# Kernel optimization log

Measured on AMD Instinct MI355X. Metric: run time of the kernel, lower is better.

The kernel has to match this reference:

```python
import jax, jax.numpy as jnp
import numpy as np

B, T, C = 4, 1024, 1024
N = 64          # head_size
H = C // N      # 16 heads
DW, DA, DV, DG = 64, 64, 64, 160


def setup_inputs() -> dict:
    key = jax.random.key(0)
    ks = iter(jax.random.split(key, 40))
    rn = lambda shape, s=1.0: jax.random.normal(next(ks), shape, dtype=jnp.float32) * s
    ru = lambda shape: jax.random.uniform(next(ks), shape, dtype=jnp.float32)
    cs = 0.5 / (C ** 0.5)
    return {
        "x": rn((B, T, C)),
        "v_first": rn((B, T, C)),
        "x_r": ru((1, 1, C)), "x_w": ru((1, 1, C)), "x_k": ru((1, 1, C)),
        "x_v": ru((1, 1, C)), "x_a": ru((1, 1, C)), "x_g": ru((1, 1, C)),
        "w0": rn((1, 1, C), 0.3) - 1.0,
        "w1": rn((C, DW), 0.05), "w2": rn((DW, C), 0.05),
        "a0": rn((1, 1, C), 0.3) - 0.19,
        "a1": rn((C, DA), 0.05), "a2": rn((DA, C), 0.05),
        "v0": rn((1, 1, C), 0.3) + 0.73,
        "v1": rn((C, DV), 0.05), "v2": rn((DV, C), 0.05),
        "g1": rn((C, DG), 0.05), "g2": rn((DG, C), 0.05),
        "k_k": ru((1, 1, C)) * 0.2 + 0.6,
        "k_a": ru((1, 1, C)) * 0.2 + 0.9,
        "r_k": rn((H, N), 0.05) - 0.04,
        "Wr": rn((C, C), cs), "Wk": rn((C, C), 0.1 * cs),
        "Wv": rn((C, C), cs), "Wo": rn((C, C), 0.02),
        "gn_w": jnp.ones((C,), jnp.float32), "gn_b": jnp.zeros((C,), jnp.float32),
        "ln_w": jnp.ones((C,), jnp.float32), "ln_b": jnp.zeros((C,), jnp.float32),
    }


def reference(x, v_first, x_r, x_w, x_k, x_v, x_a, x_g,
              w0, w1, w2, a0, a1, a2, v0, v1, v2, g1, g2,
              k_k, k_a, r_k, Wr, Wk, Wv, Wo, gn_w, gn_b, ln_w, ln_b):
    Bb, Tt, Cc = x.shape
    # ZeroPad2d((0,0,1,-1)): shift tokens right by one along T, then subtract x
    xx = jnp.concatenate([jnp.zeros_like(x[:, :1]), x[:, :-1]], axis=1) - x
    xr = x + xx * x_r; xw = x + xx * x_w; xkk = x + xx * x_k
    xv = x + xx * x_v; xa = x + xx * x_a; xg = x + xx * x_g

    r = xr @ Wr.T                                                    # [B,T,C]
    w = -jax.nn.softplus(-(w0 + jnp.tanh(xw @ w1) @ w2)) - 0.5       # log-decay <= -0.5
    k = xkk @ Wk.T
    v = xv @ Wv.T
    # layer_id=1 != 0 -> value residual mixing with v_first
    v = v + (v_first - v) * jax.nn.sigmoid(v0 + (xv @ v1) @ v2)
    a = jax.nn.sigmoid(a0 + (xa @ a1) @ a2)
    g = jax.nn.sigmoid(xg @ g1) @ g2

    kk = (k * k_k).reshape(Bb, Tt, H, N)
    kk = kk / jnp.maximum(jnp.linalg.norm(kk, axis=-1, keepdims=True), 1e-12)
    kk = kk.reshape(Bb, Tt, Cc)
    k = k * (1.0 + (a - 1.0) * k_a)

    # RWKV-7 generalized delta rule scan: kernel args (r, w, k, v, -kk, kk*a)
    decay = jnp.exp(-jnp.exp(w))                                     # [B,T,C]
    aa = -kk
    bb = kk * a
    tbhn = lambda t: t.reshape(Bb, Tt, H, N).transpose(1, 0, 2, 3)   # [T,B,H,N]
    rs, ws, ks_, vs, as_, bs = map(tbhn, (r, decay, k, v, aa, bb))

    S0 = jnp.zeros((Bb, H, N, N), dtype=x.dtype)  # [B,H, value N, key N]

    def step(S, inp):
        r_t, w_t, k_t, v_t, a_t, b_t = inp
        sa = jnp.einsum('bhij,bhj->bhi', S, a_t)                     # removal readout
        S = (S * w_t[:, :, None, :]
             + sa[..., None] * b_t[:, :, None, :]
             + v_t[..., None] * k_t[:, :, None, :])
        y = jnp.einsum('bhij,bhj->bhi', S, r_t)
        return S, (y, sa)

    _, (ys, sas) = jax.lax.scan(step, S0, (rs, ws, ks_, vs, as_, bs))
    x_att = ys.transpose(1, 0, 2, 3).reshape(Bb, Tt, Cc)
    sa_out = sas.transpose(1, 0, 2, 3).reshape(Bb, Tt, Cc)

    # ln_sa: LayerNorm over C (eps 1e-5)
    mu = sa_out.mean(-1, keepdims=True)
    var = sa_out.var(-1, keepdims=True)
    state_rep = (sa_out - mu) / jnp.sqrt(var + 1e-5) * ln_w + ln_b

    # ln_x: GroupNorm(H groups, eps=0.00064) applied per token
    xh = x_att.reshape(Bb, Tt, H, N)
    gm = xh.mean(-1, keepdims=True)
    gv = xh.var(-1, keepdims=True)
    xn = ((xh - gm) / jnp.sqrt(gv + 0.00064)).reshape(Bb, Tt, Cc) * gn_w + gn_b

    rh = r.reshape(Bb, Tt, H, N)
    kh = k.reshape(Bb, Tt, H, N)
    vh = v.reshape(Bb, Tt, H, N)
    bonus = ((rh * kh * r_k).sum(-1, keepdims=True) * vh).reshape(Bb, Tt, Cc)
    x_att = xn + bonus

    out = (x_att * g) @ Wo.T
    return out, v_first, state_rep
```

## Files before the change

kernel.cpp:

```cpp
#include <hip/hip_runtime.h>
#include <hip/hip_bf16.h>
#include <cstdint>
#include <cstddef>

typedef __attribute__((ext_vector_type(8))) short short8;
typedef __attribute__((ext_vector_type(4))) short short4v;
typedef __attribute__((ext_vector_type(4))) float f32x4;

#define DEVINL static __device__ __forceinline__

DEVINL float b2f(unsigned short u) {
    union { unsigned int i; float f; } v; v.i = ((unsigned int)u) << 16; return v.f;
}
DEVINL unsigned short f2b(float f) {
    union { float f; unsigned int i; } v; v.f = f;
    unsigned int x = v.i;
    return (unsigned short)((x + 0x7FFFu + ((x >> 16) & 1u)) >> 16);
}
DEVINL unsigned short f2bh(float f) {
    __hip_bfloat16 h = __float2bfloat16(f);
    union { __hip_bfloat16 h; unsigned short u; } v; v.h = h; return v.u;
}
DEVINL void cv8(short8 h, f32x4& lo, f32x4& hi) {
    #pragma unroll
    for (int j = 0; j < 4; ++j) {
        lo[j] = b2f((unsigned short)h[j]);
        hi[j] = b2f((unsigned short)h[j + 4]);
    }
}
DEVINL void cv4(short4v h, f32x4& o) {
    #pragma unroll
    for (int j = 0; j < 4; ++j) o[j] = b2f((unsigned short)h[j]);
}
DEVINL void stage16(const unsigned short* g, unsigned short* l) {
    __builtin_amdgcn_global_load_lds(
        (const __attribute__((address_space(1))) unsigned int*)g,
        (__attribute__((address_space(3))) unsigned int*)l,
        16, 0, 0);
}
DEVINL void xcd_swz(int& bx, int& by) {
    int id = by * 32 + bx;
    int nid = (id & 7) * 32 + (id >> 3);
    bx = nid & 31; by = nid >> 5;
}

static constexpr int Bsz = 4, Tn = 1024, Cn = 1024, Hn = 16, Nn = 64;
static constexpr int Mrows = Bsz * Tn;
static constexpr size_t MX = (size_t)Mrows * Cn;
static constexpr int NCHUNK = 16, CL = 64;
static constexpr int DLD = 65;

__global__ __launch_bounds__(256) void k_prep_all(
    const float* __restrict__ x,
    const float* __restrict__ mr, const float* __restrict__ mw,
    const float* __restrict__ mk, const float* __restrict__ mv,
    const float* __restrict__ ma, const float* __restrict__ mg,
    unsigned short* __restrict__ xr, unsigned short* __restrict__ xw,
    unsigned short* __restrict__ xk, unsigned short* __restrict__ xv,
    unsigned short* __restrict__ xa, unsigned short* __restrict__ xg,
    const float* __restrict__ Wr, const float* __restrict__ Wk,
    const float* __restrict__ Wv, const float* __restrict__ Wo,
    unsigned short* __restrict__ WrB, unsigned short* __restrict__ WkB,
    unsigned short* __restrict__ WvB, unsigned short* __restrict__ WoB,
    const float* __restrict__ w1, const float* __restrict__ w2,
    const float* __restrict__ a1, const float* __restrict__ a2,
    const float* __restrict__ v1, const float* __restrict__ v2,
    const float* __restrict__ g1, const float* __restrict__ g2,
    unsigned short* __restrict__ w1T, unsigned short* __restrict__ w2T,
    unsigned short* __restrict__ a1T, unsigned short* __restrict__ a2T,
    unsigned short* __restrict__ v1T, unsigned short* __restrict__ v2T,
    unsigned short* __restrict__ g1T, unsigned short* __restrict__ g2T)
{
    const int bx = blockIdx.x;
    const int tid = threadIdx.x;
    if (bx < 2048) {
        size_t e = ((size_t)bx * 256 + tid) * 8;
        int c = (int)(e & (Cn - 1));
        int t = (int)((e >> 10) & (Tn - 1));
        float xf[8], d[8];
        {
            f32x4 x0 = *(const f32x4*)(x + e);
            f32x4 x1 = *(const f32x4*)(x + e + 4);
            #pragma unroll
            for (int j = 0; j < 4; ++j) { xf[j] = x0[j]; xf[4 + j] = x1[j]; }
        }
        if (t > 0) {
            f32x4 p0 = *(const f32x4*)(x + e - Cn);
            f32x4 p1 = *(const f32x4*)(x + e - Cn + 4);
            #pragma unroll
            for (int j = 0; j < 4; ++j) { d[j] = p0[j] - xf[j]; d[4 + j] = p1[j] - xf[4 + j]; }
        } else {
            #pragma unroll
            for (int j = 0; j < 8; ++j) d[j] = -xf[j];
        }
        const float* ms[6] = { mr, mw, mk, mv, ma, mg };
        unsigned short* ds[6] = { xr, xw, xk, xv, xa, xg };
        #pragma unroll
        for (int p = 0; p < 6; ++p) {
            f32x4 m0 = *(const f32x4*)(ms[p] + c);
            f32x4 m1 = *(const f32x4*)(ms[p] + c + 4);
            short8 o;
            #pragma unroll
            for (int j = 0; j < 4; ++j) {
                o[j]     = (short)f2b(xf[j]     + d[j]     * m0[j]);
                o[4 + j] = (short)f2b(xf[4 + j] + d[4 + j] * m1[j]);
            }
            *(short8*)(ds[p] + e) = o;
        }
    } else if (bx < 6144) {
        int b2 = bx - 2048;
        int sel = b2 >> 10;
        const float* in = (sel == 0) ? Wr : (sel == 1) ? Wk : (sel == 2) ? Wv : Wo;
        unsigned short* out = (sel == 0) ? WrB : (sel == 1) ? WkB : (sel == 2) ? WvB : WoB;
        int i = (((b2 & 1023) << 8) + tid) * 4;
        f32x4 v = *(const f32x4*)(in + i);
        short4v o;
        #pragma unroll
        for (int j = 0; j < 4; ++j) o[j] = (short)f2b(v[j]);
        *(short4v*)(out + i) = o;
    } else {
        int idx = (bx - 6144) * 256 + tid;
        if (idx < 65536) {
            int r = idx >> 6, c = idx & 63;
            w1T[c * 1024 + r] = f2b(w1[idx]);
        } else if (idx < 131072) {
            int j = idx - 65536; int r = j >> 10, c = j & 1023;
            w2T[c * 64 + r] = f2b(w2[j]);
        } else if (idx < 196608) {
            int j = idx - 131072; int r = j >> 6, c = j & 63;
            a1T[c * 1024 + r] = f2b(a1[j]);
        } else if (idx < 262144) {
            int j = idx - 196608; int r = j >> 10, c = j & 1023;
            a2T[c * 64 + r] = f2b(a2[j]);
        } else if (idx < 327680) {
            int j = idx - 262144; int r = j >> 6, c = j & 63;
            v1T[c * 1024 + r] = f2b(v1[j]);
        } else if (idx < 393216) {
            int j = idx - 327680; int r = j >> 10, c = j & 1023;
            v2T[c * 64 + r] = f2b(v2[j]);
        } else if (idx < 557056) {
            int j = idx - 393216; int r = j / 160, c = j - r * 160;
            g1T[c * 1024 + r] = f2b(g1[j]);
        } else if (idx < 720896) {
            int j = idx - 557056; int r = j >> 10, c = j & 1023;
            g2T[c * 160 + r] = f2b(g2[j]);
        }
    }
}

template<int EPI, int OUTF32>
DEVINL void gemm_epi(f32x4 (&acc)[4][4], int m0, int n0, int N, int ldc,
                     float* Cf, unsigned short* Cb, const float* bias, int lane)
{
    int r16 = lane & 15;
    #pragma unroll
    for (int mi = 0; mi < 4; ++mi)
        #pragma unroll
        for (int ni = 0; ni < 4; ++ni) {
            int col = n0 + ni * 16 + r16;
            if (col < N) {
                float bv = (EPI >= 3) ? bias[col] : 0.f;
                #pragma unroll
                for (int r = 0; r < 4; ++r) {
                    int row = m0 + mi * 16 + (lane >> 4) * 4 + r;
                    float v = acc[mi][ni][r];
                    if (EPI == 1) v = tanhf(v);
                    else if (EPI == 2) v = 1.f / (1.f + expf(-v));
                    else if (EPI == 3) { v += bv; v = 1.f / (1.f + expf(-v)); }
                    else if (EPI == 4) { v += bv; v = expf(-0.60653066f / (1.f + expf(-v))); }
                    size_t o = (size_t)row * ldc + col;
                    if (OUTF32) Cf[o] = v; else Cb[o] = f2b(v);
                }
            }
        }
}

template<int EPI, int OUTF32>
DEVINL void gemm_lds_body(const unsigned short* __restrict__ A, int lda,
                          const unsigned short* __restrict__ Bt, int ldb,
                          float* __restrict__ Cf, unsigned short* __restrict__ Cb,
                          int ldc, const float* __restrict__ bias, int K,
                          int m0, int n0)
{
    __shared__ unsigned short As[2][128 * 32];
    __shared__ unsigned short Bs[2][128 * 32];
    const int tid = threadIdx.x, wid = tid >> 6, lane = tid & 63;
    const int r16 = lane & 15, kg = lane >> 4;
    const int wr = (wid >> 1) * 64, wc = (wid & 1) * 64;

    const int srow = wid * 32 + (lane >> 2);
    const int scol = (lane & 3) * 8;
    const int lbase = wid * 1024 + lane * 8;
    const unsigned short* aS = A + (size_t)(m0 + srow) * lda + scol;
    const unsigned short* bS = Bt + (size_t)(n0 + srow) * ldb + scol;

    f32x4 acc[4][4];
    #pragma unroll
    for (int a = 0; a < 4; ++a)
        #pragma unroll
        for (int b = 0; b < 4; ++b) acc[a][b] = (f32x4){0.f, 0.f, 0.f, 0.f};

    const int nk = K >> 5;
    stage16(aS, &As[0][lbase]);
    stage16(aS + (size_t)16 * lda, &As[0][lbase + 512]);
    stage16(bS, &Bs[0][lbase]);
    stage16(bS + (size_t)16 * ldb, &Bs[0][lbase + 512]);
    __syncthreads();

    for (int kk = 0; kk < nk; ++kk) {
        const int buf = kk & 1;
        if (kk + 1 < nk) {
            const int k0 = (kk + 1) * 32;
            stage16(aS + k0, &As[buf ^ 1][lbase]);
            stage16(aS + k0 + (size_t)16 * lda, &As[buf ^ 1][lbase + 512]);
            stage16(bS + k0, &Bs[buf ^ 1][lbase]);
            stage16(bS + k0 + (size_t)16 * ldb, &Bs[buf ^ 1][lbase + 512]);
        }
        short8 af[4], bf[4];
        #pragma unroll
        for (int mi = 0; mi < 4; ++mi)
            af[mi] = *(const short8*)&As[buf][(wr + mi * 16 + r16) * 32 + kg * 8];
        #pragma unroll
        for (int ni = 0; ni < 4; ++ni)
            bf[ni] = *(const short8*)&Bs[buf][(wc + ni * 16 + r16) * 32 + kg * 8];
        #pragma unroll
        for (int mi = 0; mi < 4; ++mi)
            #pragma unroll
            for (int ni = 0; ni < 4; ++ni)
                acc[mi][ni] = __builtin_amdgcn_mfma_f32_16x16x32_bf16(af[mi], bf[ni], acc[mi][ni], 0, 0, 0);
        __syncthreads();
    }
    gemm_epi<EPI, OUTF32>(acc, m0 + wr, n0 + wc, 1 << 30, ldc, Cf, Cb, bias, lane);
}

__global__ __launch_bounds__(256) void gemm_rkv(
    const unsigned short* __restrict__ A0, const unsigned short* __restrict__ A1,
    const unsigned short* __restrict__ A2,
    const unsigned short* __restrict__ B0, const unsigned short* __restrict__ B1,
    const unsigned short* __restrict__ B2,
    unsigned short* __restrict__ D0, unsigned short* __restrict__ D1,
    unsigned short* __restrict__ D2)
{
    int z = blockIdx.z;
    const unsigned short* A = (z == 0) ? A0 : (z == 1) ? A1 : A2;
    const unsigned short* Bt = (z == 0) ? B0 : (z == 1) ? B1 : B2;
    unsigned short* D = (z == 0) ? D0 : (z == 1) ? D1 : D2;
    int bxs = blockIdx.x, bys = blockIdx.y;
    xcd_swz(bxs, bys);
    gemm_lds_body<0, 0>(A, Cn, Bt, Cn, nullptr, D, Cn, nullptr, Cn,
                        bxs * 128, bys * 128);
}

__global__ __launch_bounds__(256) void gemm_s2(
    const unsigned short* __restrict__ hw, const unsigned short* __restrict__ ha,
    const unsigned short* __restrict__ hv, const unsigned short* __restrict__ hg,
    const unsigned short* __restrict__ w2T, const unsigned short* __restrict__ a2T,
    const unsigned short* __restrict__ v2T, const unsigned short* __restrict__ g2T,
    float* __restrict__ Wdec, unsigned short* __restrict__ Ab,
    unsigned short* __restrict__ SVb, unsigned short* __restrict__ Gb,
    const float* __restrict__ w0, const float* __restrict__ a0,
    const float* __restrict__ v0)
{
    const int z = blockIdx.z;
    int bxs = blockIdx.x, bys = blockIdx.y;
    xcd_swz(bxs, bys);
    const int m0 = bxs * 128, n0 = bys * 128;
    if (z == 0)
        gemm_lds_body<4, 1>(hw, 64, w2T, 64, Wdec, nullptr, Cn, w0, 64, m0, n0);
    else if (z == 1)
        gemm_lds_body<3, 0>(ha, 64, a2T, 64, nullptr, Ab, Cn, a0, 64, m0, n0);
    else if (z == 2)
        gemm_lds_body<3, 0>(hv, 64, v2T, 64, nullptr, SVb, Cn, v0, 64, m0, n0);
    else
        gemm_lds_body<0, 0>(hg, 160, g2T, 160, nullptr, Gb, Cn, nullptr, 160, m0, n0);
}

template<int EPI, int OUTF32>
__global__ __launch_bounds__(256) void gemm2(
    const unsigned short* __restrict__ A, int lda,
    const unsigned short* __restrict__ Bt, int ldb,
    float* __restrict__ Cf, unsigned short* __restrict__ Cb, int ldc,
    const float* __restrict__ bias, int K)
{
    int bxs = blockIdx.x, bys = blockIdx.y;
    xcd_swz(bxs, bys);
    gemm_lds_body<EPI, OUTF32>(A, lda, Bt, ldb, Cf, Cb, ldc, bias, K,
                               bxs * 128, bys * 128);
}

DEVINL void gemm_core(const unsigned short* __restrict__ A, int lda,
                      const unsigned short* __restrict__ Bt, int ldb,
                      int m0, int n0, int N, int K, int r16, int k8,
                      f32x4 (&acc)[4][4])
{
    for (int k0 = 0; k0 < K; k0 += 32) {
        short8 af[4], bf[4];
        #pragma unroll
        for (int mi = 0; mi < 4; ++mi)
            af[mi] = *(const short8*)(A + (size_t)(m0 + mi * 16 + r16) * lda + k0 + k8);
        #pragma unroll
        for (int ni = 0; ni < 4; ++ni) {
            int rn = n0 + ni * 16 + r16;
            if (rn >= N) rn = N - 1;
            bf[ni] = *(const short8*)(Bt + (size_t)rn * ldb + k0 + k8);
        }
        #pragma unroll
        for (int mi = 0; mi < 4; ++mi)
            #pragma unroll
            for (int ni = 0; ni < 4; ++ni)
                acc[mi][ni] = __builtin_amdgcn_mfma_f32_16x16x32_bf16(af[mi], bf[ni], acc[mi][ni], 0, 0, 0);
    }
}

__global__ __launch_bounds__(256) void gemm_small1(
    const unsigned short* __restrict__ Aw, const unsigned short* __restrict__ Aa,
    const unsigned short* __restrict__ Av, const unsigned short* __restrict__ Ag,
    const unsigned short* __restrict__ Bw, const unsigned short* __restrict__ Ba,
    const unsigned short* __restrict__ Bv, const unsigned short* __restrict__ Bg,
    unsigned short* __restrict__ Dw, unsigned short* __restrict__ Da,
    unsigned short* __restrict__ Dv, unsigned short* __restrict__ Dg)
{
    int z = blockIdx.z;
    if (z < 3 && blockIdx.y > 0) return;
    const unsigned short* A = (z == 0) ? Aw : (z == 1) ? Aa : (z == 2) ? Av : Ag;
    const unsigned short* Bt = (z == 0) ? Bw : (z == 1) ? Ba : (z == 2) ? Bv : Bg;
    const int N = (z == 3) ? 160 : 64;
    const int tid = threadIdx.x, wid = tid >> 6, lane = tid & 63;
    const int r16 = lane & 15, k8 = (lane >> 4) * 8;
    const int m0 = blockIdx.x * 256 + wid * 64;
    const int n0 = blockIdx.y * 64;
    f32x4 acc[4][4];
    #pragma unroll
    for (int a = 0; a < 4; ++a)
        #pragma unroll
        for (int b = 0; b < 4; ++b) acc[a][b] = (f32x4){0.f, 0.f, 0.f, 0.f};
    gemm_core(A, Cn, Bt, Cn, m0, n0, N, Cn, r16, k8, acc);
    if (z == 0)      gemm_epi<1, 0>(acc, m0, n0, N, 64,  nullptr, Dw, nullptr, lane);
    else if (z == 1) gemm_epi<0, 0>(acc, m0, n0, N, 64,  nullptr, Da, nullptr, lane);
    else if (z == 2) gemm_epi<0, 0>(acc, m0, n0, N, 64,  nullptr, Dv, nullptr, lane);
    else             gemm_epi<2, 0>(acc, m0, n0, N, 160, nullptr, Dg, nullptr, lane);
}

__global__ __launch_bounds__(1024, 1) void kA_wy(
    const float* __restrict__ Wp,
    unsigned short* __restrict__ Kp,
    unsigned short* __restrict__ Vp,
    const unsigned short* __restrict__ SVp,
    unsigned short* __restrict__ Aap,
    const float* __restrict__ vfirst,
    const float* __restrict__ kkw, const float* __restrict__ kaw,
    float* __restrict__ Pg,
    float* __restrict__ Cg,
    float* __restrict__ Qg,
    float* __restrict__ SAp)
{
    __shared__ float Dl[64 * DLD];
    __shared__ float Lf[64 * 72];
    __shared__ float Xf[64 * 132];
    __shared__ unsigned short ah[64 * 72], al[64 * 72];
    __shared__ unsigned short bh_[64 * 72], bl_[64 * 72];
    __shared__ unsigned short kh[64 * 72], kl[64 * 72];
    __shared__ unsigned short vt[64 * 72];
    __shared__ unsigned short sc[64 * 72];
    __shared__ float dT[64];

    const int tid = threadIdx.x;
    const int bx = blockIdx.x;
    const int bhd = bx >> 4, cc = bx & 15;
    const size_t base0 = ((size_t)(bhd >> 4) * Tn + (size_t)cc * CL) * Cn + (size_t)(bhd & 15) * Nn;
    const size_t mb = (size_t)bx * 4096;

    {
        const int t = tid >> 4, s4 = (tid & 15) * 4;
        const size_t g = base0 + (size_t)t * Cn + s4;
        const int ch = (bhd & 15) * Nn + s4;

        f32x4 kv, av, vv, sv;
        cv4(*(const short4v*)(Kp + g), kv);
        cv4(*(const short4v*)(Aap + g), av);
        cv4(*(const short4v*)(Vp + g), vv);
        cv4(*(const short4v*)(SVp + g), sv);
        f32x4 kkwv = *(const f32x4*)(kkw + ch);
        f32x4 kawv = *(const f32x4*)(kaw + ch);
        f32x4 vfv  = *(const f32x4*)(vfirst + g);

        f32x4 kkv = kv * kkwv;
        f32x4 sq = kkv * kkv;
        float s = sq[0] + sq[1] + sq[2] + sq[3];
        s += __shfl_xor(s, 1, 64); s += __shfl_xor(s, 2, 64);
        s += __shfl_xor(s, 4, 64); s += __shfl_xor(s, 8, 64);
        float inv = 1.f / fmaxf(sqrtf(s), 1e-12f);

        short4v o_a, o_b, o_k, o_v;
        #pragma unroll
        for (int j = 0; j < 4; ++j) {
            float kkx = kkv[j] * inv;
            o_a[j] = (short)f2b(-kkx);
            o_b[j] = (short)f2b(kkx * av[j]);
            float kf = kv[j] * (1.f + (av[j] - 1.f) * kawv[j]);
            o_k[j] = (short)f2b(kf);
            float vf = vv[j] + (vfv[j] - vv[j]) * sv[j];
            o_v[j] = (short)f2b(vf);
        }
        *(short4v*)&ah[t * 72 + s4] = o_a;
        *(short4v*)&bh_[t * 72 + s4] = o_b;
        *(short4v*)&kh[t * 72 + s4] = o_k;
        *(short4v*)&sc[t * 72 + s4] = o_v;
        *(short4v*)(Kp + g) = o_k;
        *(short4v*)(Vp + g) = o_v;
        *(short4v*)(Aap + g) = o_b;
    }
    __syncthreads();

    float wreg[4];
    {
        const int j = tid & 63, seg = tid >> 6;
        const float* wp = Wp + base0 + (size_t)(seg * 4) * Cn + j;
        float run = 1.f;
        #pragma unroll
        for (int u = 0; u < 4; ++u) { wreg[u] = wp[(size_t)u * Cn]; run *= wreg[u]; }
        Xf[seg * 64 + j] = run;
    }
    __syncthreads();
    {
        const int j = tid & 63, seg = tid >> 6;
        float d = 1.f;
        for (int q = 0; q < seg; ++q) d *= Xf[q * 64 + j];
        #pragma unroll
        for (int u = 0; u < 4; ++u) { d *= wreg[u]; Dl[(seg * 4 + u) * DLD + j] = d; }
        if (seg == 15) dT[j] = d;
    }
    __syncthreads();

    {
        const int t = tid >> 4, s4 = (tid & 15) * 4;
        short4v a4 = *(const short4v*)&ah[t * 72 + s4];
        short4v b4 = *(const short4v*)&bh_[t * 72 + s4];
        short4v k4 = *(const short4v*)&kh[t * 72 + s4];
        short4v oah, oal, obh, obl, okh, okl;
        #pragma unroll
        for (int jj = 0; jj < 4; ++jj) {
            const int j = s4 + jj;
            const float Dt = Dl[t * DLD + j];
            const float Dp = (t == 0) ? 1.f : Dl[(t - 1) * DLD + j];
            const float inv = __builtin_amdgcn_rcpf(Dt);
            float av = b2f((unsigned short)a4[jj]) * Dp;
            unsigned short h = f2bh(av);
            oah[jj] = (short)h; oal[jj] = (short)f2bh(av - b2f(h));
            float bv = b2f((unsigned short)b4[jj]) * inv;
            h = f2bh(bv);
            obh[jj] = (short)h; obl[jj] = (short)f2bh(bv - b2f(h));
            float kv = b2f((unsigned short)k4[jj]) * inv;
            h = f2bh(kv);
            okh[jj] = (short)h; okl[jj] = (short)f2bh(kv - b2f(h));
        }
        *(short4v*)&ah[t * 72 + s4] = oah;  *(short4v*)&al[t * 72 + s4] = oal;
        *(short4v*)&bh_[t * 72 + s4] = obh; *(short4v*)&bl_[t * 72 + s4] = obl;
        *(short4v*)&kh[t * 72 + s4] = okh;  *(short4v*)&kl[t * 72 + s4] = okl;
    }
    {
        const int rj = tid & 63, tq = tid >> 6;
        short4v ov;
        #pragma unroll
        for (int u = 0; u < 4; ++u)
            ov[u] = (short)sc[(tq * 4 + u) * 72 + rj];
        *(short4v*)&vt[rj * 72 + tq * 4] = ov;
    }
    __syncthreads();

    const int w = tid >> 6, lane = tid & 63;
    const int r16 = lane & 15, kg = lane >> 4;
    const int rt = w >> 2, ct = w & 3;

    {
        if (ct > rt) {
            #pragma unroll
            for (int r = 0; r < 4; ++r)
                sc[(rt * 16 + kg * 4 + r) * 72 + ct * 16 + r16] = 0;
        } else {
            short8 Ah[2], Al2[2];
            #pragma unroll
            for (int ks = 0; ks < 2; ++ks) {
                Ah[ks]  = *(const short8*)&ah[(rt * 16 + r16) * 72 + ks * 32 + kg * 8];
                Al2[ks] = *(const short8*)&al[(rt * 16 + r16) * 72 + ks * 32 + kg * 8];
            }
            f32x4 aL = (f32x4){0.f, 0.f, 0.f, 0.f};
            f32x4 aK = (f32x4){0.f, 0.f, 0.f, 0.f};
            #pragma unroll
            for (int ks = 0; ks < 2; ++ks) {
                const int so = (ct * 16 + r16) * 72 + ks * 32 + kg * 8;
                short8 Bh = *(const short8*)&bh_[so];
                short8 Bl = *(const short8*)&bl_[so];
                aL = __builtin_amdgcn_mfma_f32_16x16x32_bf16(Ah[ks], Bh, aL, 0, 0, 0);
                aL = __builtin_amdgcn_mfma_f32_16x16x32_bf16(Ah[ks], Bl, aL, 0, 0, 0);
                aL = __builtin_amdgcn_mfma_f32_16x16x32_bf16(Al2[ks], Bh, aL, 0, 0, 0);
                short8 Kh2 = *(const short8*)&kh[so];
                short8 Kl2 = *(const short8*)&kl[so];
                aK = __builtin_amdgcn_mfma_f32_16x16x32_bf16(Ah[ks], Kh2, aK, 0, 0, 0);
                aK = __builtin_amdgcn_mfma_f32_16x16x32_bf16(Ah[ks], Kl2, aK, 0, 0, 0);
                aK = __builtin_amdgcn_mfma_f32_16x16x32_bf16(Al2[ks], Kh2, aK, 0, 0, 0);
            }
            #pragma unroll
            for (int r = 0; r < 4; ++r) {
                const int t = rt * 16 + kg * 4 + r;
                const int s = ct * 16 + r16;
                Lf[t * 72 + s] = (s < t) ? aL[r] : 0.f;
                sc[t * 72 + s] = (s < t) ? f2bh(aK[r]) : (unsigned short)0;
            }
        }
    }
    __syncthreads();

    {
        const int t = tid >> 4, s4 = (tid & 15) * 4;
        #pragma unroll
        for (int jj = 0; jj < 4; ++jj)
            Xf[t * 132 + s4 + jj] = b2f(ah[t * 72 + s4 + jj]) + b2f(al[t * 72 + s4 + jj]);
    }
    {
        f32x4 acc = (f32x4){0.f, 0.f, 0.f, 0.f};
        #pragma unroll
        for (int ks = 0; ks < 2; ++ks) {
            short8 Af = *(const short8*)&sc[(rt * 16 + r16) * 72 + ks * 32 + kg * 8];
            short8 Bf = *(const short8*)&vt[(ct * 16 + r16) * 72 + ks * 32 + kg * 8];
            acc = __builtin_amdgcn_mfma_f32_16x16x32_bf16(Af, Bf, acc, 0, 0, 0);
        }
        #pragma unroll
        for (int r = 0; r < 4; ++r)
            Xf[(rt * 16 + kg * 4 + r) * 132 + 64 + ct * 16 + r16] = acc[r];
    }
    __syncthreads();

    for (int bi = 0; bi < 4; ++bi) {
        if (bi > 0) {
            const int c = tid & 127;
            const int rb = tid >> 7;
            const int t0 = bi * 16 + rb * 2;
            float a0 = Xf[t0 * 132 + c];
            float a1 = Xf[(t0 + 1) * 132 + c];
            for (int s = 0; s < bi * 16; ++s) {
                float xv = Xf[s * 132 + c];
                a0 += Lf[t0 * 72 + s] * xv;
                a1 += Lf[(t0 + 1) * 72 + s] * xv;
            }
            Xf[t0 * 132 + c] = a0;
            Xf[(t0 + 1) * 132 + c] = a1;
            __syncthreads();
        }
        if (w < 2) {
            const int c = w * 64 + lane;
            float xcol[16];
            #pragma unroll
            for (int u = 0; u < 16; ++u) xcol[u] = Xf[(bi * 16 + u) * 132 + c];
            for (int rr = 1; rr < 16; ++rr) {
                float a2 = xcol[rr];
                for (int s = 0; s < rr; ++s)
                    a2 += Lf[(bi * 16 + rr) * 72 + bi * 16 + s] * xcol[s];
                xcol[rr] = a2;
            }
            #pragma unroll
            for (int u = 1; u < 16; ++u) Xf[(bi * 16 + u) * 132 + c] = xcol[u];
        }
        __syncthreads();
    }

    {
        const int rj = tid & 63, tq = tid >> 6;
        float qv[4], sv[4];
        unsigned short bhv[4], blv[4], khv[4], klv[4];
        #pragma unroll
        for (int u = 0; u < 4; ++u) {
            const int t = tq * 4 + u;
            qv[u] = Xf[t * 132 + rj];
            sv[u] = Xf[t * 132 + 64 + rj];
            bhv[u] = bh_[t * 72 + rj];
            blv[u] = bl_[t * 72 + rj];
            khv[u] = kh[t * 72 + rj];
            klv[u] = kl[t * 72 + rj];
        }
        #pragma unroll
        for (int u = 0; u < 4; ++u) {
            const int t = tq * 4 + u;
            Qg[mb + (size_t)t * 64 + rj] = qv[u];
            SAp[base0 + (size_t)t * Cn + rj] = sv[u];
        }
        __syncthreads();
        unsigned short* sath = (unsigned short*)Lf;
        unsigned short* satl = ((unsigned short*)Lf) + 64 * 72;
        short4v oqh, oql, osh, osl, obh, obl, okh, okl;
        #pragma unroll
        for (int u = 0; u < 4; ++u) {
            unsigned short h = f2bh(qv[u]);
            oqh[u] = (short)h; oql[u] = (short)f2bh(qv[u] - b2f(h));
            h = f2bh(sv[u]);
            osh[u] = (short)h; osl[u] = (short)f2bh(sv[u] - b2f(h));
            obh[u] = (short)bhv[u]; obl[u] = (short)blv[u];
            okh[u] = (short)khv[u]; okl[u] = (short)klv[u];
        }
        *(short4v*)&ah[rj * 72 + tq * 4] = oqh;
        *(short4v*)&al[rj * 72 + tq * 4] = oql;
        *(short4v*)&sath[rj * 72 + tq * 4] = osh;
        *(short4v*)&satl[rj * 72 + tq * 4] = osl;
        *(short4v*)&bh_[rj * 72 + tq * 4] = obh;
        *(short4v*)&bl_[rj * 72 + tq * 4] = obl;
        *(short4v*)&kh[rj * 72 + tq * 4] = okh;
        *(short4v*)&kl[rj * 72 + tq * 4] = okl;
    }
    __syncthreads();

    {
        unsigned short* sath = (unsigned short*)Lf;
        unsigned short* satl = ((unsigned short*)Lf) + 64 * 72;
        f32x4 aP = (f32x4){0.f, 0.f, 0.f, 0.f};
        f32x4 aC = (f32x4){0.f, 0.f, 0.f, 0.f};
        #pragma unroll
        for (int ks = 0; ks < 2; ++ks) {
            const int ro = (rt * 16 + r16) * 72 + ks * 32 + kg * 8;
            const int co = (ct * 16 + r16) * 72 + ks * 32 + kg * 8;
            short8 Abh = *(const short8*)&bh_[ro];
            short8 Abl = *(const short8*)&bl_[ro];
            short8 Bqh = *(const short8*)&ah[co];
            short8 Bql = *(const short8*)&al[co];
            aP = __builtin_amdgcn_mfma_f32_16x16x32_bf16(Abh, Bqh, aP, 0, 0, 0);
            aP = __builtin_amdgcn_mfma_f32_16x16x32_bf16(Abh, Bql, aP, 0, 0, 0);
            aP = __builtin_amdgcn_mfma_f32_16x16x32_bf16(Abl, Bqh, aP, 0, 0, 0);
            short8 Ash = *(const short8*)&sath[ro];
            short8 Asl = *(const short8*)&satl[ro];
            short8 Bbh = *(const short8*)&bh_[co];
            short8 Bbl = *(const short8*)&bl_[co];
            aC = __builtin_amdgcn_mfma_f32_16x16x32_bf16(Ash, Bbh, aC, 0, 0, 0);
            aC = __builtin_amdgcn_mfma_f32_16x16x32_bf16(Ash, Bbl, aC, 0, 0, 0);
            aC = __builtin_amdgcn_mfma_f32_16x16x32_bf16(Asl, Bbh, aC, 0, 0, 0);
            short8 Avt = *(const short8*)&vt[ro];
            short8 Bkh = *(const short8*)&kh[co];
            short8 Bkl = *(const short8*)&kl[co];
            aC = __builtin_amdgcn_mfma_f32_16x16x32_bf16(Avt, Bkh, aC, 0, 0, 0);
            aC = __builtin_amdgcn_mfma_f32_16x16x32_bf16(Avt, Bkl, aC, 0, 0, 0);
        }
        #pragma unroll
        for (int r = 0; r < 4; ++r) {
            const int row = rt * 16 + kg * 4 + r;
            const int col = ct * 16 + r16;
            Pg[mb + (size_t)row * 64 + col] = dT[row] * (aP[r] + ((row == col) ? 1.f : 0.f));
            Cg[mb + (size_t)row * 64 + col] = dT[col] * aC[r];
        }
    }
}

__global__ __launch_bounds__(256, 1) void kB_combine(
    const float* __restrict__ Pg, const float* __restrict__ Cg,
    float* __restrict__ Sinit)
{
    __shared__ float Sl[64 * 65];
    __shared__ float PT[64 * 65];
    const int tid = threadIdx.x;
    const int w = tid >> 6;
    const int l = tid & 63;
    const int lr = l & 15;
    const int lg = l >> 4;
    const int bh = blockIdx.x;

    f32x4 acc[4];
    #pragma unroll
    for (int t = 0; t < 4; ++t) acc[t] = (f32x4){0.f, 0.f, 0.f, 0.f};

    f32x4 pr[4]; f32x4 cr[4];
    {
        const size_t ob = (size_t)(bh * 16) * 4096;
        #pragma unroll
        for (int u = 0; u < 4; ++u)
            pr[u] = *(const f32x4*)(Pg + ob + (size_t)tid * 16 + u * 4);
        #pragma unroll
        for (int t = 0; t < 4; ++t)
            #pragma unroll
            for (int r = 0; r < 4; ++r)
                cr[t][r] = Cg[ob + (size_t)(16 * w + 4 * lg + r) * 64 + 16 * t + lr];
    }

    for (int c = 0; c < NCHUNK; ++c) {
        const size_t ob = (size_t)(bh * 16 + c) * 4096;
        #pragma unroll
        for (int t = 0; t < 4; ++t)
            #pragma unroll
            for (int r = 0; r < 4; ++r)
                Sinit[ob + (size_t)(16 * w + 4 * lg + r) * 64 + 16 * t + lr] = acc[t][r];
        if (c == NCHUNK - 1) break;

        #pragma unroll
        for (int t = 0; t < 4; ++t)
            #pragma unroll
            for (int r = 0; r < 4; ++r)
                Sl[(16 * w + 4 * lg + r) * 65 + 16 * t + lr] = acc[t][r];
        {
            const int jr = tid >> 2, j0 = (tid & 3) * 16;
            #pragma unroll
            for (int u = 0; u < 4; ++u)
                #pragma unroll
                for (int e = 0; e < 4; ++e)
                    PT[jr * 65 + j0 + u * 4 + e] = pr[u][e];
        }
        __syncthreads();

        f32x4 prn[4] = {}, crn[4] = {};
        if (c + 1 < NCHUNK - 1) {
            const size_t obn = (size_t)(bh * 16 + c + 1) * 4096;
            #pragma unroll
            for (int u = 0; u < 4; ++u)
                prn[u] = *(const f32x4*)(Pg + obn + (size_t)tid * 16 + u * 4);
            #pragma unroll
            for (int t = 0; t < 4; ++t)
                #pragma unroll
                for (int r = 0; r < 4; ++r)
                    crn[t][r] = Cg[obn + (size_t)(16 * w + 4 * lg + r) * 64 + 16 * t + lr];
        }

        short8 ahi[2], alo[2];
        #pragma unroll
        for (int k0 = 0; k0 < 2; ++k0) {
            const float* sp = &Sl[(16 * w + lr) * 65 + k0 * 32 + lg * 8];
            #pragma unroll
            for (int j = 0; j < 8; ++j) {
                float s = sp[j];
                unsigned short h = f2bh(s);
                ahi[k0][j] = (short)h;
                alo[k0][j] = (short)f2bh(s - b2f(h));
            }
        }

        #pragma unroll
        for (int t = 0; t < 4; ++t) {
            f32x4 nacc = cr[t];
            #pragma unroll
            for (int k0 = 0; k0 < 2; ++k0) {
                short8 bhi, blo;
                const float* pp = &PT[(16 * t + lr) * 65 + k0 * 32 + lg * 8];
                #pragma unroll
                for (int j = 0; j < 8; ++j) {
                    float p = pp[j];
                    unsigned short h = f2bh(p);
                    bhi[j] = (short)h;
                    blo[j] = (short)f2bh(p - b2f(h));
                }
                nacc = __builtin_amdgcn_mfma_f32_16x16x32_bf16(ahi[k0], bhi, nacc, 0, 0, 0);
                nacc = __builtin_amdgcn_mfma_f32_16x16x32_bf16(ahi[k0], blo, nacc, 0, 0, 0);
                nacc = __builtin_amdgcn_mfma_f32_16x16x32_bf16(alo[k0], bhi, nacc, 0, 0, 0);
            }
            acc[t] = nacc;
        }
        __syncthreads();
        #pragma unroll
        for (int u = 0; u < 4; ++u) { pr[u] = prn[u]; cr[u] = crn[u]; }
    }
}

__global__ __launch_bounds__(256) void kY_mfma(
    const float* __restrict__ Wp, const unsigned short* __restrict__ Rp,
    const unsigned short* __restrict__ Kp, const unsigned short* __restrict__ Bbp,
    const unsigned short* __restrict__ Vp,
    const float* __restrict__ Qg, const float* __restrict__ Sinit,
    float* __restrict__ SAp,
    float* __restrict__ Yp)
{
    __shared__ float Dl[64 * DLD];
    __shared__ unsigned short khS[64 * 72], klS[64 * 72];
    __shared__ unsigned short bhS[64 * 72], blS[64 * 72];
    __shared__ unsigned short vtS[64 * 72];
    __shared__ unsigned short sahS[64 * 72];

    unsigned short* scoreS = (unsigned short*)Dl;
    float* SAf = Dl;
    float* segP = (float*)vtS;

    const int tid = threadIdx.x;
    const int bx = blockIdx.x;
    const int bh = bx >> 4, cc = bx & 15;
    const size_t base0 = ((size_t)(bh >> 4) * Tn + (size_t)cc * CL) * Cn + (size_t)(bh & 15) * Nn;
    const size_t mb = (size_t)bx * 4096;

    float wv[16];
    {
        const int j = tid & 63, seg = tid >> 6;
        float run = 1.f;
        #pragma unroll
        for (int u = 0; u < 16; ++u) {
            wv[u] = Wp[base0 + (size_t)(seg * 16 + u) * Cn + j];
            run *= wv[u];
        }
        segP[seg * 64 + j] = run;
    }
    __syncthreads();
    {
        const int j = tid & 63, seg = tid >> 6;
        float d = 1.f;
        for (int q = 0; q < seg; ++q) d *= segP[q * 64 + j];
        #pragma unroll
        for (int u = 0; u < 16; ++u) {
            d *= wv[u];
            Dl[(seg * 16 + u) * DLD + j] = d;
        }
    }
    __syncthreads();

    const int w = tid >> 6, lane = tid & 63;
    const int r16 = lane & 15, kg = lane >> 4;

    short8 rh[2], rl[2];
    {
        const int t = 16 * w + r16;
        #pragma unroll
        for (int ks = 0; ks < 2; ++ks) {
            const int j0 = ks * 32 + kg * 8;
            short8 rr = *(const short8*)(Rp + base0 + (size_t)t * Cn + j0);
            const float* dp = &Dl[t * DLD + j0];
            #pragma unroll
            for (int jj = 0; jj < 8; ++jj) {
                float rv = b2f((unsigned short)rr[jj]) * dp[jj];
                unsigned short h = f2bh(rv);
                rh[ks][jj] = (short)h;
                rl[ks][jj] = (short)f2bh(rv - b2f(h));
            }
        }
    }

    {
        const int s = tid >> 2, j0 = (tid & 3) * 16;
        const size_t g = base0 + (size_t)s * Cn + j0;
        #pragma unroll
        for (int half = 0; half < 2; ++half) {
            short8 kk8 = *(const short8*)(Kp + g + half * 8);
            short8 bb8 = *(const short8*)(Bbp + g + half * 8);
            short8 okh, okl, obh, obl;
            #pragma unroll
            for (int jj = 0; jj < 8; ++jj) {
                float dd = Dl[s * DLD + j0 + half * 8 + jj];
                float inv = __builtin_amdgcn_rcpf(dd);
                float kv = b2f((unsigned short)kk8[jj]) * inv;
                float bv = b2f((unsigned short)bb8[jj]) * inv;
                unsigned short h1 = f2bh(kv);
                okh[jj] = (short)h1; okl[jj] = (short)f2bh(kv - b2f(h1));
                unsigned short h2 = f2bh(bv);
                obh[jj] = (short)h2; obl[jj] = (short)f2bh(bv - b2f(h2));
            }
            *(short8*)&khS[s * 72 + j0 + half * 8] = okh;
            *(short8*)&klS[s * 72 + j0 + half * 8] = okl;
            *(short8*)&bhS[s * 72 + j0 + half * 8] = obh;
            *(short8*)&blS[s * 72 + j0 + half * 8] = obl;
            *(short8*)&sahS[s * 72 + j0 + half * 8] =
                *(const short8*)(Vp + g + half * 8);
        }
    }
    __syncthreads();

    {
        const int rj = tid & 63, tq = tid >> 6;
        unsigned short tmp[16];
        #pragma unroll
        for (int u = 0; u < 16; ++u)
            tmp[u] = sahS[(tq * 16 + u) * 72 + rj];
        short8 o0, o1;
        #pragma unroll
        for (int u = 0; u < 8; ++u) { o0[u] = (short)tmp[u]; o1[u] = (short)tmp[8 + u]; }
        *(short8*)&vtS[rj * 72 + tq * 16] = o0;
        *(short8*)&vtS[rj * 72 + tq * 16 + 8] = o1;
    }
    __syncthreads();

    f32x4 acc[4], accC[4];
    #pragma unroll
    for (int ni = 0; ni < 4; ++ni) {
        acc[ni] = (f32x4){0.f, 0.f, 0.f, 0.f};
        accC[ni] = (f32x4){0.f, 0.f, 0.f, 0.f};
    }
    short8 qh[2], ql[2];
    if (cc > 0) {
        const int t = 16 * w + r16;
        #pragma unroll
        for (int ks = 0; ks < 2; ++ks) {
            const int j0 = ks * 32 + kg * 8;
            f32x4 qa = *(const f32x4*)(Qg + mb + (size_t)t * 64 + j0);
            f32x4 qb = *(const f32x4*)(Qg + mb + (size_t)t * 64 + j0 + 4);
            #pragma unroll
            for (int jj = 0; jj < 4; ++jj) {
                unsigned short h1 = f2bh(qa[jj]);
                qh[ks][jj] = (short)h1; ql[ks][jj] = (short)f2bh(qa[jj] - b2f(h1));
                unsigned short h2 = f2bh(qb[jj]);
                qh[ks][4 + jj] = (short)h2; ql[ks][4 + jj] = (short)f2bh(qb[jj] - b2f(h2));
            }
        }
    }
    #pragma unroll
    for (int ni = 0; ni < 4; ++ni) {
        #pragma unroll
        for (int ks = 0; ks < 2; ++ks) {
            const int i = ni * 16 + r16;
            const int j0 = ks * 32 + kg * 8;
            f32x4 s0a = *(const f32x4*)(Sinit + mb + (size_t)i * 64 + j0);
            f32x4 s0b = *(const f32x4*)(Sinit + mb + (size_t)i * 64 + j0 + 4);
            short8 s0h, s0l;
            #pragma unroll
            for (int jj = 0; jj < 4; ++jj) {
                unsigned short h1 = f2bh(s0a[jj]);
                s0h[jj] = (short)h1; s0l[jj] = (short)f2bh(s0a[jj] - b2f(h1));
                unsigned short h2 = f2bh(s0b[jj]);
                s0h[4 + jj] = (short)h2; s0l[4 + jj] = (short)f2bh(s0b[jj] - b2f(h2));
            }
            acc[ni] = __builtin_amdgcn_mfma_f32_16x16x32_bf16(rh[ks], s0h, acc[ni], 0, 0, 0);
            acc[ni] = __builtin_amdgcn_mfma_f32_16x16x32_bf16(rh[ks], s0l, acc[ni], 0, 0, 0);
            acc[ni] = __builtin_amdgcn_mfma_f32_16x16x32_bf16(rl[ks], s0h, acc[ni], 0, 0, 0);
            if (cc > 0) {
                accC[ni] = __builtin_amdgcn_mfma_f32_16x16x32_bf16(qh[ks], s0h, accC[ni], 0, 0, 0);
                accC[ni] = __builtin_amdgcn_mfma_f32_16x16x32_bf16(qh[ks], s0l, accC[ni], 0, 0, 0);
                accC[ni] = __builtin_amdgcn_mfma_f32_16x16x32_bf16(ql[ks], s0h, accC[ni], 0, 0, 0);
            }
        }
    }

    #pragma unroll
    for (int ni = 0; ni < 4; ++ni) {
        #pragma unroll
        for (int r = 0; r < 4; ++r) {
            const int t = 16 * w + kg * 4 + r;
            const int i = ni * 16 + r16;
            const size_t off = base0 + (size_t)t * Cn + i;
            float sa = SAp[off] + accC[ni][r];
            SAp[off] = sa;
            SAf[t * 65 + i] = sa;
        }
    }
    __syncthreads();

    {
        const int rj = tid & 63, tq = tid >> 6;
        unsigned short tmp[16];
        #pragma unroll
        for (int u = 0; u < 16; ++u)
            tmp[u] = f2bh(SAf[(tq * 16 + u) * 65 + rj]);
        short8 o0, o1;
        #pragma unroll
        for (int u = 0; u < 8; ++u) { o0[u] = (short)tmp[u]; o1[u] = (short)tmp[8 + u]; }
        *(short8*)&sahS[rj * 72 + tq * 16] = o0;
        *(short8*)&sahS[rj * 72 + tq * 16 + 8] = o1;
    }
    __syncthreads();

    #pragma unroll
    for (int si = 0; si < 4; ++si) {
        f32x4 sc2 = (f32x4){0.f, 0.f, 0.f, 0.f};
        #pragma unroll
        for (int ks = 0; ks < 2; ++ks) {
            const int srow = si * 16 + r16;
            const int j0 = ks * 32 + kg * 8;
            short8 kbh = *(const short8*)&khS[srow * 72 + j0];
            short8 kbl = *(const short8*)&klS[srow * 72 + j0];
            sc2 = __builtin_amdgcn_mfma_f32_16x16x32_bf16(rh[ks], kbh, sc2, 0, 0, 0);
            sc2 = __builtin_amdgcn_mfma_f32_16x16x32_bf16(rh[ks], kbl, sc2, 0, 0, 0);
            sc2 = __builtin_amdgcn_mfma_f32_16x16x32_bf16(rl[ks], kbh, sc2, 0, 0, 0);
        }
        const int s = si * 16 + r16;
        #pragma unroll
        for (int r = 0; r < 4; ++r) {
            const int t = 16 * w + kg * 4 + r;
            scoreS[t * 72 + s] = (s <= t) ? f2bh(sc2[r]) : (unsigned short)0;
        }
    }
    #pragma unroll
    for (int ni = 0; ni < 4; ++ni) {
        #pragma unroll
        for (int ks = 0; ks < 2; ++ks) {
            short8 af = *(const short8*)&scoreS[(16 * w + r16) * 72 + ks * 32 + kg * 8];
            short8 vf = *(const short8*)&vtS[(ni * 16 + r16) * 72 + ks * 32 + kg * 8];
            acc[ni] = __builtin_amdgcn_mfma_f32_16x16x32_bf16(af, vf, acc[ni], 0, 0, 0);
        }
    }
    __syncthreads();

    #pragma unroll
    for (int si = 0; si < 4; ++si) {
        f32x4 sc2 = (f32x4){0.f, 0.f, 0.f, 0.f};
        #pragma unroll
        for (int ks = 0; ks < 2; ++ks) {
            const int srow = si * 16 + r16;
            const int j0 = ks * 32 + kg * 8;
            short8 bbh = *(const short8*)&bhS[srow * 72 + j0];
            short8 bbl = *(const short8*)&blS[srow * 72 + j0];
            sc2 = __builtin_amdgcn_mfma_f32_16x16x32_bf16(rh[ks], bbh, sc2, 0, 0, 0);
            sc2 = __builtin_amdgcn_mfma_f32_16x16x32_bf16(rh[ks], bbl, sc2, 0, 0, 0);
            sc2 = __builtin_amdgcn_mfma_f32_16x16x32_bf16(rl[ks], bbh, sc2, 0, 0, 0);
        }
        const int s = si * 16 + r16;
        #pragma unroll
        for (int r = 0; r < 4; ++r) {
            const int t = 16 * w + kg * 4 + r;
            scoreS[t * 72 + s] = (s <= t) ? f2bh(sc2[r]) : (unsigned short)0;
        }
    }
    #pragma unroll
    for (int ni = 0; ni < 4; ++ni) {
        #pragma unroll
        for (int ks = 0; ks < 2; ++ks) {
            short8 af = *(const short8*)&scoreS[(16 * w + r16) * 72 + ks * 32 + kg * 8];
            short8 sh = *(const short8*)&sahS[(ni * 16 + r16) * 72 + ks * 32 + kg * 8];
            acc[ni] = __builtin_amdgcn_mfma_f32_16x16x32_bf16(af, sh, acc[ni], 0, 0, 0);
        }
    }

    #pragma unroll
    for (int ni = 0; ni < 4; ++ni) {
        #pragma unroll
        for (int r = 0; r < 4; ++r) {
            const int t = 16 * w + kg * 4 + r;
            Yp[base0 + (size_t)t * Cn + ni * 16 + r16] = acc[ni][r];
        }
    }
}

__global__ __launch_bounds__(256) void k_elem2(
    const float* __restrict__ Yb, const unsigned short* __restrict__ Rb,
    const unsigned short* __restrict__ Kb, const unsigned short* __restrict__ Vb,
    const unsigned short* __restrict__ Gb,
    const float* __restrict__ gnw, const float* __restrict__ gnb,
    const float* __restrict__ rk,
    unsigned short* __restrict__ AG)
{
    int tid = threadIdx.x;
    size_t gh = (size_t)blockIdx.x * 4 + (tid >> 6);
    int lane = tid & 63;
    int h = (int)(gh & (Hn - 1));
    size_t idx = (gh >> 4) * Cn + (size_t)h * Nn + lane;
    int c = h * Nn + lane;

    float y = Yb[idx];
    float s1 = y, s2 = y * y;
    float p = b2f(Rb[idx]) * b2f(Kb[idx]) * rk[c];
    #pragma unroll
    for (int m = 1; m < 64; m <<= 1) {
        s1 += __shfl_xor(s1, m, 64);
        s2 += __shfl_xor(s2, m, 64);
        p  += __shfl_xor(p, m, 64);
    }
    float mean = s1 * (1.f / 64.f);
    float var = s2 * (1.f / 64.f) - mean * mean;
    float xn = (y - mean) * rsqrtf(var + 0.00064f) * gnw[c] + gnb[c];
    float xatt = xn + p * b2f(Vb[idx]);
    AG[idx] = f2b(xatt * b2f(Gb[idx]));
}

__global__ __launch_bounds__(256) void k_ln(
    const float* __restrict__ SAp,
    const float* __restrict__ lnw, const float* __restrict__ lnb,
    const float* __restrict__ vf_in, float* __restrict__ vf_out,
    float* __restrict__ outp)
{
    __shared__ float red1[4], red2[4];
    int tid = threadIdx.x;
    size_t row = blockIdx.x;
    *(f32x4*)(vf_out + row * Cn + tid * 4) = *(const f32x4*)(vf_in + row * Cn + tid * 4);

    f32x4 v = *(const f32x4*)(SAp + row * Cn + tid * 4);
    float s1 = v[0] + v[1] + v[2] + v[3];
    float s2 = v[0] * v[0] + v[1] * v[1] + v[2] * v[2] + v[3] * v[3];
    #pragma unroll
    for (int m = 1; m < 64; m <<= 1) {
        s1 += __shfl_xor(s1, m, 64);
        s2 += __shfl_xor(s2, m, 64);
    }
    if ((tid & 63) == 0) { red1[tid >> 6] = s1; red2[tid >> 6] = s2; }
    __syncthreads();
    s1 = red1[0] + red1[1] + red1[2] + red1[3];
    s2 = red2[0] + red2[1] + red2[2] + red2[3];
    float mean = s1 * (1.f / 1024.f);
    float var = s2 * (1.f / 1024.f) - mean * mean;
    float rs = rsqrtf(var + 1e-5f);
    f32x4 o;
    #pragma unroll
    for (int u = 0; u < 4; ++u) {
        int c = tid * 4 + u;
        o[u] = (v[u] - mean) * rs * lnw[c] + lnb[c];
    }
    *(f32x4*)(outp + row * Cn + tid * 4) = o;
}

extern "C" void kernel_launch(void* const* d_in, const int* in_sizes, int n_in,
                              void* d_out, int out_size, void* d_ws, size_t ws_size,
                              hipStream_t stream)
{
    (void)in_sizes; (void)n_in; (void)out_size; (void)ws_size;
    const float* x      = (const float*)d_in[0];
    const float* vfirst = (const float*)d_in[1];
    const float* x_r    = (const float*)d_in[2];
    const float* x_w    = (const float*)d_in[3];
    const float* x_k    = (const float*)d_in[4];
    const float* x_v    = (const float*)d_in[5];
    const float* x_a    = (const float*)d_in[6];
    const float* x_g    = (const float*)d_in[7];
    const float* w0     = (const float*)d_in[8];
    const float* w1     = (const float*)d_in[9];
    const float* w2     = (const float*)d_in[10];
    const float* a0     = (const float*)d_in[11];
    const float* a1     = (const float*)d_in[12];
    const float* a2     = (const float*)d_in[13];
    const float* v0     = (const float*)d_in[14];
    const float* v1     = (const float*)d_in[15];
    const float* v2     = (const float*)d_in[16];
    const float* g1     = (const float*)d_in[17];
    const float* g2     = (const float*)d_in[18];
    const float* k_k    = (const float*)d_in[19];
    const float* k_a    = (const float*)d_in[20];
    const float* r_k    = (const float*)d_in[21];
    const float* Wr     = (const float*)d_in[22];
    const float* Wk     = (const float*)d_in[23];
    const float* Wv     = (const float*)d_in[24];
    const float* Wo     = (const float*)d_in[25];
    const float* gn_w   = (const float*)d_in[26];
    const float* gn_b   = (const float*)d_in[27];
    const float* ln_w   = (const float*)d_in[28];
    const float* ln_b   = (const float*)d_in[29];

    char* ws = (char*)d_ws;
    size_t off = 0;
    auto alloc = [&](size_t bytes) -> void* {
        void* p = ws + off;
        off += (bytes + 255) & ~(size_t)255;
        return p;
    };
    unsigned short* Rb  = (unsigned short*)alloc(MX * 2);
    unsigned short* Kb  = (unsigned short*)alloc(MX * 2);
    unsigned short* Vb  = (unsigned short*)alloc(MX * 2);
    unsigned short* SVb = (unsigned short*)alloc(MX * 2);
    unsigned short* Ab  = (unsigned short*)alloc(MX * 2);
    unsigned short* Gb  = (unsigned short*)alloc(MX * 2);
    float* Wdec = (float*)alloc(MX * 4);
    float* Cg   = (float*)alloc(MX * 4);
    float* Pg   = (float*)alloc(MX * 4);
    float* Qg   = (float*)alloc(MX * 4);
    unsigned short* hw = (unsigned short*)alloc((size_t)Mrows * 64 * 2);
    unsigned short* ha = (unsigned short*)alloc((size_t)Mrows * 64 * 2);
    unsigned short* hv = (unsigned short*)alloc((size_t)Mrows * 64 * 2);
    unsigned short* hg = (unsigned short*)alloc((size_t)Mrows * 160 * 2);
    unsigned short* WrB = (unsigned short*)alloc(1048576 * 2);
    unsigned short* WkB = (unsigned short*)alloc(1048576 * 2);
    unsigned short* WvB = (unsigned short*)alloc(1048576 * 2);
    unsigned short* WoB = (unsigned short*)alloc(1048576 * 2);
    unsigned short* w1T = (unsigned short*)alloc(65536 * 2);
    unsigned short* w2T = (unsigned short*)alloc(65536 * 2);
    unsigned short* a1T = (unsigned short*)alloc(65536 * 2);
    unsigned short* a2T = (unsigned short*)alloc(65536 * 2);
    unsigned short* v1T = (unsigned short*)alloc(65536 * 2);
    unsigned short* v2T = (unsigned short*)alloc(65536 * 2);
    unsigned short* g1T = (unsigned short*)alloc(163840 * 2);
    unsigned short* g2T = (unsigned short*)alloc(163840 * 2);

    unsigned short* xrB = (unsigned short*)Cg;
    unsigned short* xkB = (unsigned short*)Cg + MX;
    unsigned short* xvB = (unsigned short*)Wdec;
    unsigned short* xgB = (unsigned short*)Wdec + MX;
    unsigned short* xwB = Ab;
    unsigned short* xaB = Gb;

    float* out_o  = (float*)d_out;
    float* out_vf = out_o + MX;
    float* out_sr = out_o + 2 * MX;
    float* Sinit = out_vf;
    float* Yb    = out_o;
    float* SAb   = out_sr;
    unsigned short* AG = Rb;

    k_prep_all<<<dim3(8960), 256, 0, stream>>>(
        x, x_r, x_w, x_k, x_v, x_a, x_g,
        xrB, xwB, xkB, xvB, xaB, xgB,
        Wr, Wk, Wv, Wo, WrB, WkB, WvB, WoB,
        w1, w2, a1, a2, v1, v2, g1, g2,
        w1T, w2T, a1T, a2T, v1T, v2T, g1T, g2T);

    gemm_small1<<<dim3(16, 3, 4), 256, 0, stream>>>(xwB, xaB, xvB, xgB,
                                                    w1T, a1T, v1T, g1T,
                                                    hw, ha, hv, hg);
    gemm_rkv<<<dim3(32, 8, 3), 256, 0, stream>>>(xrB, xkB, xvB, WrB, WkB, WvB,
                                                 Rb, Kb, Vb);

    gemm_s2<<<dim3(32, 8, 4), 256, 0, stream>>>(hw, ha, hv, hg,
                                                w2T, a2T, v2T, g2T,
                                                Wdec, Ab, SVb, Gb,
                                                w0, a0, v0);

    kA_wy<<<dim3(1024), 1024, 0, stream>>>(Wdec, Kb, Vb, SVb, Ab,
                                           vfirst, k_k, k_a,
                                           Pg, Cg, Qg, SAb);
    kB_combine<<<dim3(64), 256, 0, stream>>>(Pg, Cg, Sinit);
    kY_mfma<<<dim3(1024), 256, 0, stream>>>(Wdec, Rb, Kb, Ab, Vb,
                                            Qg, Sinit, SAb, Yb);

    k_elem2<<<dim3(16384), 256, 0, stream>>>(Yb, Rb, Kb, Vb, Gb, gn_w, gn_b, r_k, AG);

    k_ln<<<dim3(4096), 256, 0, stream>>>(SAb, ln_w, ln_b, vfirst, out_vf, out_sr);
    gemm2<0, 1><<<dim3(32, 8), 256, 0, stream>>>(AG, Cn, WoB, Cn, out_o, nullptr, Cn, nullptr, Cn);
}
```

Baseline: 320.5 us.

## Fuse GroupNorm, bonus and gate epilogue into kY_mfma and drop k_elem2

The per-token GroupNorm, r·k·r_k bonus and sigmoid-gate multiply are moved into the kY_mfma epilogue. They now work directly on the MFMA accumulators, using 16-lane shuffles for the head reductions and reading v from the shared-memory vtS tile. This removes the fp32 Y round trip through global memory and the separate k_elem2 launch. The risks are that vtS must still hold valid v at that point, and that AG aliases Rb, which the same kernel reads just before writing.

```diff
diff --git a/kernel.cpp b/kernel.cpp
--- a/kernel.cpp
+++ b/kernel.cpp
@@ -756,10 +756,12 @@
 __global__ __launch_bounds__(256) void kY_mfma(
     const float* __restrict__ Wp, const unsigned short* __restrict__ Rp,
     const unsigned short* __restrict__ Kp, const unsigned short* __restrict__ Bbp,
-    const unsigned short* __restrict__ Vp,
+    const unsigned short* __restrict__ Vp, const unsigned short* __restrict__ Gb,
     const float* __restrict__ Qg, const float* __restrict__ Sinit,
+    const float* __restrict__ gnw, const float* __restrict__ gnb,
+    const float* __restrict__ rk,
     float* __restrict__ SAp,
-    float* __restrict__ Yp)
+    unsigned short* __restrict__ AG)
 {
     __shared__ float Dl[64 * DLD];
     __shared__ unsigned short khS[64 * 72], klS[64 * 72];
@@ -1004,45 +1006,48 @@
         }
     }
 
-    #pragma unroll
-    for (int ni = 0; ni < 4; ++ni) {
+    {
+        const int hh = bh & 15;
+        float rkv[4], gnwv[4], gnbv[4];
+        #pragma unroll
+        for (int ni = 0; ni < 4; ++ni) {
+            const int c = hh * 64 + ni * 16 + r16;
+            rkv[ni] = rk[c]; gnwv[ni] = gnw[c]; gnbv[ni] = gnb[c];
+        }
         #pragma unroll
         for (int r = 0; r < 4; ++r) {
             const int t = 16 * w + kg * 4 + r;
-            Yp[base0 + (size_t)t * Cn + ni * 16 + r16] = acc[ni][r];
-        }
-    }
-}
-
-__global__ __launch_bounds__(256) void k_elem2(
-    const float* __restrict__ Yb, const unsigned short* __restrict__ Rb,
-    const unsigned short* __restrict__ Kb, const unsigned short* __restrict__ Vb,
-    const unsigned short* __restrict__ Gb,
-    const float* __restrict__ gnw, const float* __restrict__ gnb,
-    const float* __restrict__ rk,
-    unsigned short* __restrict__ AG)
-{
-    int tid = threadIdx.x;
-    size_t gh = (size_t)blockIdx.x * 4 + (tid >> 6);
-    int lane = tid & 63;
-    int h = (int)(gh & (Hn - 1));
-    size_t idx = (gh >> 4) * Cn + (size_t)h * Nn + lane;
-    int c = h * Nn + lane;
-
-    float y = Yb[idx];
-    float s1 = y, s2 = y * y;
-    float p = b2f(Rb[idx]) * b2f(Kb[idx]) * rk[c];
-    #pragma unroll
-    for (int m = 1; m < 64; m <<= 1) {
-        s1 += __shfl_xor(s1, m, 64);
-        s2 += __shfl_xor(s2, m, 64);
-        p  += __shfl_xor(p, m, 64);
-    }
-    float mean = s1 * (1.f / 64.f);
-    float var = s2 * (1.f / 64.f) - mean * mean;
-    float xn = (y - mean) * rsqrtf(var + 0.00064f) * gnw[c] + gnb[c];
-    float xatt = xn + p * b2f(Vb[idx]);
-    AG[idx] = f2b(xatt * b2f(Gb[idx]));
+            const size_t rowb = base0 + (size_t)t * Cn;
+            float s1 = 0.f, s2 = 0.f, p = 0.f;
+            float yv[4];
+            #pragma unroll
+            for (int ni = 0; ni < 4; ++ni) {
+                float y = acc[ni][r];
+                yv[ni] = y;
+                s1 += y; s2 += y * y;
+                const int i = ni * 16 + r16;
+                p += b2f(Rp[rowb + i]) * b2f(Kp[rowb + i]) * rkv[ni];
+            }
+            s1 += __shfl_xor(s1, 1, 64); s1 += __shfl_xor(s1, 2, 64);
+            s1 += __shfl_xor(s1, 4, 64); s1 += __shfl_xor(s1, 8, 64);
+            s2 += __shfl_xor(s2, 1, 64); s2 += __shfl_xor(s2, 2, 64);
+            s2 += __shfl_xor(s2, 4, 64); s2 += __shfl_xor(s2, 8, 64);
+            p  += __shfl_xor(p, 1, 64);  p  += __shfl_xor(p, 2, 64);
+            p  += __shfl_xor(p, 4, 64);  p  += __shfl_xor(p, 8, 64);
+            float mean = s1 * (1.f / 64.f);
+            float var = s2 * (1.f / 64.f) - mean * mean;
+            float rs = rsqrtf(var + 0.00064f);
+            #pragma unroll
+            for (int ni = 0; ni < 4; ++ni) {
+                const int i = ni * 16 + r16;
+                float xn = (yv[ni] - mean) * rs * gnwv[ni] + gnbv[ni];
+                float vv2 = b2f(vtS[i * 72 + t]);
+                float xatt = xn + p * vv2;
+                float gv = b2f(Gb[rowb + i]);
+                AG[rowb + i] = f2b(xatt * gv);
+            }
+        }
+    }
 }
 
 __global__ __launch_bounds__(256) void k_ln(
@@ -1161,7 +1166,6 @@
     float* out_vf = out_o + MX;
     float* out_sr = out_o + 2 * MX;
     float* Sinit = out_vf;
-    float* Yb    = out_o;
     float* SAb   = out_sr;
     unsigned short* AG = Rb;
 
@@ -1187,10 +1191,9 @@
                                            vfirst, k_k, k_a,
                                            Pg, Cg, Qg, SAb);
     kB_combine<<<dim3(64), 256, 0, stream>>>(Pg, Cg, Sinit);
-    kY_mfma<<<dim3(1024), 256, 0, stream>>>(Wdec, Rb, Kb, Ab, Vb,
-                                            Qg, Sinit, SAb, Yb);
-
-    k_elem2<<<dim3(16384), 256, 0, stream>>>(Yb, Rb, Kb, Vb, Gb, gn_w, gn_b, r_k, AG);
+    kY_mfma<<<dim3(1024), 256, 0, stream>>>(Wdec, Rb, Kb, Ab, Vb, Gb,
+                                            Qg, Sinit, gn_w, gn_b, r_k,
+                                            SAb, AG);
 
     k_ln<<<dim3(4096), 256, 0, stream>>>(SAb, ln_w, ln_b, vfirst, out_vf, out_sr);
     gemm2<0, 1><<<dim3(32, 8), 256, 0, stream>>>(AG, Cn, WoB, Cn, out_o, nullptr, Cn, nullptr, Cn);
```

Result: faster. 307.8 us (-4.0%).
